# Performance work log

Hardware: AMD Instinct MI355X
Metric: run time of the kernel (lower is better)

## Reference

```python
import jax, jax.numpy as jnp
import numpy as np

BSZ, P, D, C = 16, 4096, 256, 512


def setup_inputs() -> dict:
    key = jax.random.key(0)
    k1, k2 = jax.random.split(key)
    x = jax.random.normal(k1, (BSZ, P, D), dtype=jnp.float32)
    kernels = jax.random.normal(k2, (C, D), dtype=jnp.float32) * 0.001
    return {"x": x, "kernels": kernels}


def reference(x, kernels):
    bsz, Pn, d = x.shape
    # (bsz, P, C) projection scores, ReLU'd
    scores = jax.nn.relu(jnp.einsum('bpd,cd->bpc', x, kernels))
    # per-channel argmax over positions -> (bsz, C)
    idx = jnp.argmax(scores, axis=1)
    # scatter_add each kernel row into its winning position
    b_idx = jnp.arange(bsz)[:, None]  # (bsz, 1) broadcast against (bsz, C)
    src = jnp.broadcast_to(kernels, (bsz,) + kernels.shape)  # (bsz, C, d)
    out = jnp.zeros((bsz, Pn, d), dtype=x.dtype).at[b_idx, idx].add(src)
    return out
```

## Files before the change

kernel.cpp:

```cpp
#include <hip/hip_runtime.h>
#include <cstddef>
#include <cstdint>

#define BSZ 16
#define PN  4096
#define DD  256
#define CC  512
#define TP  128
#define TC  64
#define NPT (PN / TP)
#define NCT (CC / TC)
#define NKC 8

typedef short bf16x8 __attribute__((ext_vector_type(8)));
typedef float f32x4  __attribute__((ext_vector_type(4)));

#define MEMFENCE() __asm__ __volatile__("" ::: "memory")
#define WAITCNT_VM0 0x1F70

struct Top2 { float v1, v2; int i1, i2; };

__device__ __forceinline__ void t2_insert(Top2& t, float v, int i) {
  if (v > t.v1 || (v == t.v1 && i < t.i1)) {
    t.v2 = t.v1; t.i2 = t.i1; t.v1 = v; t.i1 = i;
  } else if (v > t.v2 || (v == t.v2 && i < t.i2)) {
    t.v2 = v; t.i2 = i;
  }
}

__device__ __forceinline__ void split4(float4 v, uint2& hp, uint2& lp) {
  uint32_t u0 = __float_as_uint(v.x), u1 = __float_as_uint(v.y),
           u2 = __float_as_uint(v.z), u3 = __float_as_uint(v.w);
  float l0 = v.x - __uint_as_float(u0 & 0xffff0000u);
  float l1 = v.y - __uint_as_float(u1 & 0xffff0000u);
  float l2 = v.z - __uint_as_float(u2 & 0xffff0000u);
  float l3 = v.w - __uint_as_float(u3 & 0xffff0000u);
  hp.x = __builtin_amdgcn_perm(u1, u0, 0x07060302u);
  hp.y = __builtin_amdgcn_perm(u3, u2, 0x07060302u);
  lp.x = __builtin_amdgcn_perm(__float_as_uint(l1), __float_as_uint(l0), 0x07060302u);
  lp.y = __builtin_amdgcn_perm(__float_as_uint(l3), __float_as_uint(l2), 0x07060302u);
}

__device__ __forceinline__ void gld16(const void* gsrc, void* ldst) {
  __builtin_amdgcn_global_load_lds(
      (const __attribute__((address_space(1))) unsigned int*)gsrc,
      (__attribute__((address_space(3))) unsigned int*)ldst, 16, 0, 0);
}

__global__ __launch_bounds__(256) void convert_k_kernel(
    const float* __restrict__ kern, uint32_t* __restrict__ ks) {
  const int kc = blockIdx.x, ct = blockIdx.y;
  const size_t chunk = ((size_t)ct * NKC + kc) * 4096;
#pragma unroll
  for (int s0 = 0; s0 < 2; s0++) {
    int s  = threadIdx.x + s0 * 256;
    int fp = s >> 6, kg = (s >> 4) & 3, lr = s & 15;
    int r  = fp * 16 + lr, k0 = kg * 8;
    const float* src = kern + ((size_t)ct * 128 + r) * DD + kc * 32 + k0;
    float4 v0 = *(const float4*)src, v1 = *(const float4*)(src + 4);
    uint2 h0, l0, h1, l1; split4(v0, h0, l0); split4(v1, h1, l1);
    *(uint4*)&ks[chunk + (size_t)s * 4]        = make_uint4(h0.x, h0.y, h1.x, h1.y);
    *(uint4*)&ks[chunk + 2048 + (size_t)s * 4] = make_uint4(l0.x, l0.y, l1.x, l1.y);
  }
}

__global__ __launch_bounds__(256, 4) void score_kernel(
    const float* __restrict__ x, const uint32_t* __restrict__ ks,
    float2* __restrict__ pv2, uint32_t* __restrict__ pix) {

  __shared__ __align__(16) char lds[16384];

  const int d  = blockIdx.x;
  const int L  = (d & 7) * 512 + (d >> 3);
  const int ct = L & 7;
  const int pt = (L >> 3) & 31;
  const int b  = L >> 8;

  const int tid = threadIdx.x;
  const int lane = tid & 63, w = tid >> 6;
  const int lr = lane & 15, kg = lane >> 4;

  const char* ksbase = (const char*)ks + (size_t)(ct >> 1) * NKC * 16384 + (ct & 1) * 4096;
  const char* bsrc[2];
  bsrc[0] = ksbase + tid * 16;
  bsrc[1] = ksbase + 8192 + tid * 16;

  const char* xbase = (const char*)(x + ((size_t)b * PN + (size_t)pt * TP) * DD);
  const char* ap[2][2];
#pragma unroll
  for (int fp = 0; fp < 2; fp++)
#pragma unroll
    for (int h = 0; h < 2; h++)
      ap[fp][h] = xbase + (size_t)(w * 32 + fp * 16 + lr) * (DD * 4) + kg * 32 + h * 16;

  float4 abuf[2][2][2];

  auto issue = [&](int kc) {
    char* Bb = lds + (kc & 1) * 8192;
#pragma unroll
    for (int i = 0; i < 2; i++)
      gld16(bsrc[i] + kc * 16384, Bb + i * 4096 + tid * 16);
#pragma unroll
    for (int fp = 0; fp < 2; fp++)
#pragma unroll
      for (int h = 0; h < 2; h++)
        abuf[kc & 1][fp][h] = *(const float4*)(ap[fp][h] + kc * 128);
  };

  issue(0);
  MEMFENCE();
  __builtin_amdgcn_s_waitcnt(WAITCNT_VM0);
  __builtin_amdgcn_s_barrier();
  MEMFENCE();

  f32x4 acc[2][4];
#pragma unroll
  for (int i = 0; i < 2; i++)
#pragma unroll
    for (int j = 0; j < 4; j++) acc[i][j] = (f32x4)0.f;

#pragma unroll
  for (int kc = 0; kc < NKC; kc++) {
    if (kc + 1 < NKC) issue(kc + 1);

    bf16x8 Ah[2], Al[2];
#pragma unroll
    for (int fp = 0; fp < 2; fp++) {
      uint2 h0, l0, h1, l1;
      split4(abuf[kc & 1][fp][0], h0, l0);
      split4(abuf[kc & 1][fp][1], h1, l1);
      uint4 hh = make_uint4(h0.x, h0.y, h1.x, h1.y);
      uint4 ll = make_uint4(l0.x, l0.y, l1.x, l1.y);
      Ah[fp] = *(bf16x8*)&hh;
      Al[fp] = *(bf16x8*)&ll;
    }
    const char* Bb = lds + (kc & 1) * 8192;
#pragma unroll
    for (int fc = 0; fc < 4; fc++) {
      bf16x8 Bh = *(const bf16x8*)(Bb + fc * 1024 + lane * 16);
      bf16x8 Bl = *(const bf16x8*)(Bb + 4096 + fc * 1024 + lane * 16);
#pragma unroll
      for (int fp = 0; fp < 2; fp++) {
        acc[fp][fc] = __builtin_amdgcn_mfma_f32_16x16x32_bf16(Ah[fp], Bh, acc[fp][fc], 0, 0, 0);
        acc[fp][fc] = __builtin_amdgcn_mfma_f32_16x16x32_bf16(Ah[fp], Bl, acc[fp][fc], 0, 0, 0);
        acc[fp][fc] = __builtin_amdgcn_mfma_f32_16x16x32_bf16(Al[fp], Bh, acc[fp][fc], 0, 0, 0);
      }
    }
    MEMFENCE();
    __builtin_amdgcn_s_waitcnt(WAITCNT_VM0);
    __builtin_amdgcn_s_barrier();
    MEMFENCE();
  }

  float4* scratch = (float4*)lds;
  const int slot = w * 4 + kg;
#pragma unroll
  for (int fc = 0; fc < 4; fc++) {
    Top2 t; t.v1 = -1.f; t.v2 = -1.f; t.i1 = 0x7fffffff; t.i2 = 0x7fffffff;
#pragma unroll
    for (int fp = 0; fp < 2; fp++)
#pragma unroll
      for (int r = 0; r < 4; r++) {
        float v = acc[fp][fc][r]; v = v > 0.f ? v : 0.f;
        t2_insert(t, v, w * 32 + fp * 16 + kg * 4 + r);
      }
    scratch[slot * TC + fc * 16 + lr] =
        make_float4(t.v1, __int_as_float(t.i1), t.v2, __int_as_float(t.i2));
  }
  __syncthreads();

  if (tid < TC) {
    Top2 t; t.v1 = -1.f; t.v2 = -1.f; t.i1 = 0x7fffffff; t.i2 = 0x7fffffff;
#pragma unroll
    for (int s = 0; s < 16; s++) {
      float4 e = scratch[s * TC + tid];
      t2_insert(t, e.x, __float_as_int(e.y));
      t2_insert(t, e.z, __float_as_int(e.w));
    }
    int c = ct * TC + tid;
    size_t o = ((size_t)b * CC + c) * NPT + pt;
    uint32_t p1 = (uint32_t)(pt * TP + t.i1);
    uint32_t p2 = (uint32_t)(pt * TP + t.i2);
    pv2[o] = make_float2(t.v1, t.v2);
    pix[o] = (p1 << 16) | (p2 & 0xffffu);
  }
}

__global__ __launch_bounds__(64) void reduce_winner_kernel(
    const float2* __restrict__ pv2, const uint32_t* __restrict__ pix,
    const float* __restrict__ x, const float* __restrict__ kern,
    int* __restrict__ winner) {
  const int c = blockIdx.x, b = blockIdx.y;
  const int l = threadIdx.x;

  Top2 t; t.v1 = -1.f; t.v2 = -1.f; t.i1 = 0x7fffffff; t.i2 = 0x7fffffff;
  if (l < NPT) {
    size_t o = ((size_t)b * CC + c) * NPT + l;
    float2 v = pv2[o]; uint32_t ii = pix[o];
    t.v1 = v.x; t.v2 = v.y; t.i1 = (int)(ii >> 16); t.i2 = (int)(ii & 0xffffu);
  }
#pragma unroll
  for (int m = 1; m < 64; m <<= 1) {
    float uv1 = __shfl_xor(t.v1, m, 64);
    int   ui1 = __shfl_xor(t.i1, m, 64);
    float uv2 = __shfl_xor(t.v2, m, 64);
    int   ui2 = __shfl_xor(t.i2, m, 64);
    t2_insert(t, uv1, ui1);
    t2_insert(t, uv2, ui2);
  }

  int win = t.i1;
  if (t.v1 - t.v2 <= 1e-4f * t.v1 + 1e-5f) {
    const float4* x1 = (const float4*)(x + ((size_t)b * PN + t.i1) * DD);
    const float4* x2 = (const float4*)(x + ((size_t)b * PN + t.i2) * DD);
    const float4* kc = (const float4*)(kern + (size_t)c * DD);
    float4 a1 = x1[l], a2 = x2[l], k4 = kc[l];
    float s1 = a1.x * k4.x + a1.y * k4.y + a1.z * k4.z + a1.w * k4.w;
    float s2 = a2.x * k4.x + a2.y * k4.y + a2.z * k4.z + a2.w * k4.w;
#pragma unroll
    for (int m = 1; m < 64; m <<= 1) {
      s1 += __shfl_xor(s1, m, 64);
      s2 += __shfl_xor(s2, m, 64);
    }
    s1 = fmaxf(s1, 0.f); s2 = fmaxf(s2, 0.f);
    if (s2 > s1 || (s2 == s1 && t.i2 < t.i1)) win = t.i2;
  }
  if (l == 0) winner[(size_t)b * CC + c] = win;
}

__global__ __launch_bounds__(256) void write_out_kernel(
    const int* __restrict__ winner, const float* __restrict__ kern,
    float4* __restrict__ out) {
  __shared__ __align__(16) int wrow[CC];
  const int b = blockIdx.y;
  const int tid = threadIdx.x, lane = tid & 63, w = tid >> 6;
  const int p = blockIdx.x * 4 + w;

  *(int2*)&wrow[tid * 2] = *(const int2*)&winner[(size_t)b * CC + tid * 2];
  __syncthreads();

  int4 w0 = *(const int4*)&wrow[lane * 8];
  int4 w1 = *(const int4*)&wrow[lane * 8 + 4];
  int wv[8] = {w0.x, w0.y, w0.z, w0.w, w1.x, w1.y, w1.z, w1.w};

  float4 acc = make_float4(0.f, 0.f, 0.f, 0.f);
#pragma unroll
  for (int j = 0; j < 8; j++) {
    unsigned long long m = __ballot(wv[j] == p);
    while (m) {
      int bit = __ffsll((long long)m) - 1; m &= m - 1;
      int c = bit * 8 + j;
      float4 kv = ((const float4*)(kern + (size_t)c * DD))[lane];
      acc.x += kv.x; acc.y += kv.y; acc.z += kv.z; acc.w += kv.w;
    }
  }
  out[((size_t)b * PN + p) * 64 + lane] = acc;
}

extern "C" void kernel_launch(void* const* d_in, const int* in_sizes, int n_in,
                              void* d_out, int out_size, void* d_ws, size_t ws_size,
                              hipStream_t stream) {
  const float* x    = (const float*)d_in[0];
  const float* kern = (const float*)d_in[1];
  float* out = (float*)d_out;

  char* ws = (char*)d_ws;
  float2*   pv2 = (float2*)ws;
  uint32_t* pix = (uint32_t*)(ws + (size_t)BSZ * CC * NPT * sizeof(float2));
  uint32_t* ks  = (uint32_t*)(ws + 3u * 1024 * 1024);
  int*      win = (int*)(ws + 3u * 1024 * 1024 + 512u * 1024);

  convert_k_kernel<<<dim3(NKC, CC / 128), 256, 0, stream>>>(kern, ks);

  score_kernel<<<dim3(NCT * NPT * BSZ), 256, 0, stream>>>(x, ks, pv2, pix);

  reduce_winner_kernel<<<dim3(CC, BSZ), 64, 0, stream>>>(pv2, pix, x, kern, win);

  write_out_kernel<<<dim3(PN / 4, BSZ), 256, 0, stream>>>(win, kern, (float4*)out);
}
```

Before: 196.2 us.

## Double score tile height, triple-buffer B in LDS, and widen reduce blocks

Doubles the position tile in the score kernel to 256 rows, so each wave computes 64 rows and every B fragment read from LDS feeds twice as many MFMAs. It also splits the A register prefetch from the B LDS prefetch, triple-buffers B two chunks ahead with partial vmcnt waits, and raises wave priority around the MFMA block. The reduce kernel now packs four channels per 256-thread block, and the convert kernel spreads its work across a third grid dimension. The cost is more accumulator registers (launch bounds drop to 2 blocks per SM) and half as many score blocks, which may lower occupancy and load balance.

```diff
diff --git a/kernel.cpp b/kernel.cpp
--- a/kernel.cpp
+++ b/kernel.cpp
@@ -6,7 +6,7 @@
 #define PN  4096
 #define DD  256
 #define CC  512
-#define TP  128
+#define TP  256
 #define TC  64
 #define NPT (PN / TP)
 #define NCT (CC / TC)
@@ -17,6 +17,7 @@
 
 #define MEMFENCE() __asm__ __volatile__("" ::: "memory")
 #define WAITCNT_VM0 0x1F70
+#define WAITCNT_VM2 0x1F72
 
 struct Top2 { float v1, v2; int i1, i2; };
 
@@ -51,30 +52,27 @@
     const float* __restrict__ kern, uint32_t* __restrict__ ks) {
   const int kc = blockIdx.x, ct = blockIdx.y;
   const size_t chunk = ((size_t)ct * NKC + kc) * 4096;
-#pragma unroll
-  for (int s0 = 0; s0 < 2; s0++) {
-    int s  = threadIdx.x + s0 * 256;
-    int fp = s >> 6, kg = (s >> 4) & 3, lr = s & 15;
-    int r  = fp * 16 + lr, k0 = kg * 8;
-    const float* src = kern + ((size_t)ct * 128 + r) * DD + kc * 32 + k0;
-    float4 v0 = *(const float4*)src, v1 = *(const float4*)(src + 4);
-    uint2 h0, l0, h1, l1; split4(v0, h0, l0); split4(v1, h1, l1);
-    *(uint4*)&ks[chunk + (size_t)s * 4]        = make_uint4(h0.x, h0.y, h1.x, h1.y);
-    *(uint4*)&ks[chunk + 2048 + (size_t)s * 4] = make_uint4(l0.x, l0.y, l1.x, l1.y);
-  }
-}
-
-__global__ __launch_bounds__(256, 4) void score_kernel(
+  int s  = threadIdx.x + blockIdx.z * 256;
+  int fp = s >> 6, kg = (s >> 4) & 3, lr = s & 15;
+  int r  = fp * 16 + lr, k0 = kg * 8;
+  const float* src = kern + ((size_t)ct * 128 + r) * DD + kc * 32 + k0;
+  float4 v0 = *(const float4*)src, v1 = *(const float4*)(src + 4);
+  uint2 h0, l0, h1, l1; split4(v0, h0, l0); split4(v1, h1, l1);
+  *(uint4*)&ks[chunk + (size_t)s * 4]        = make_uint4(h0.x, h0.y, h1.x, h1.y);
+  *(uint4*)&ks[chunk + 2048 + (size_t)s * 4] = make_uint4(l0.x, l0.y, l1.x, l1.y);
+}
+
+__global__ __launch_bounds__(256, 2) void score_kernel(
     const float* __restrict__ x, const uint32_t* __restrict__ ks,
     float2* __restrict__ pv2, uint32_t* __restrict__ pix) {
 
-  __shared__ __align__(16) char lds[16384];
+  __shared__ __align__(16) char lds[24576];
 
   const int d  = blockIdx.x;
-  const int L  = (d & 7) * 512 + (d >> 3);
+  const int L  = (d & 7) * 256 + (d >> 3);
   const int ct = L & 7;
-  const int pt = (L >> 3) & 31;
-  const int b  = L >> 8;
+  const int pt = (L >> 3) & 15;
+  const int b  = L >> 7;
 
   const int tid = threadIdx.x;
   const int lane = tid & 63, w = tid >> 6;
@@ -86,46 +84,52 @@
   bsrc[1] = ksbase + 8192 + tid * 16;
 
   const char* xbase = (const char*)(x + ((size_t)b * PN + (size_t)pt * TP) * DD);
-  const char* ap[2][2];
-#pragma unroll
-  for (int fp = 0; fp < 2; fp++)
+  const char* ap[4][2];
+#pragma unroll
+  for (int fp = 0; fp < 4; fp++)
 #pragma unroll
     for (int h = 0; h < 2; h++)
-      ap[fp][h] = xbase + (size_t)(w * 32 + fp * 16 + lr) * (DD * 4) + kg * 32 + h * 16;
-
-  float4 abuf[2][2][2];
-
-  auto issue = [&](int kc) {
-    char* Bb = lds + (kc & 1) * 8192;
-#pragma unroll
-    for (int i = 0; i < 2; i++)
-      gld16(bsrc[i] + kc * 16384, Bb + i * 4096 + tid * 16);
-#pragma unroll
-    for (int fp = 0; fp < 2; fp++)
+      ap[fp][h] = xbase + (size_t)(w * 64 + fp * 16 + lr) * (DD * 4) + kg * 32 + h * 16;
+
+  float4 abuf[2][4][2];
+
+  auto loadA = [&](int kc) {
+#pragma unroll
+    for (int fp = 0; fp < 4; fp++)
 #pragma unroll
       for (int h = 0; h < 2; h++)
         abuf[kc & 1][fp][h] = *(const float4*)(ap[fp][h] + kc * 128);
   };
-
-  issue(0);
+  auto issueB = [&](int kc) {
+    char* Bb = lds + (kc % 3) * 8192;
+#pragma unroll
+    for (int i = 0; i < 2; i++)
+      gld16(bsrc[i] + kc * 16384, Bb + i * 4096 + tid * 16);
+  };
+
+  loadA(0);
+  issueB(0);
+  issueB(1);
   MEMFENCE();
-  __builtin_amdgcn_s_waitcnt(WAITCNT_VM0);
+  __builtin_amdgcn_s_waitcnt(WAITCNT_VM2);
   __builtin_amdgcn_s_barrier();
   MEMFENCE();
 
-  f32x4 acc[2][4];
-#pragma unroll
-  for (int i = 0; i < 2; i++)
+  f32x4 acc[4][4];
+#pragma unroll
+  for (int i = 0; i < 4; i++)
 #pragma unroll
     for (int j = 0; j < 4; j++) acc[i][j] = (f32x4)0.f;
 
 #pragma unroll
   for (int kc = 0; kc < NKC; kc++) {
-    if (kc + 1 < NKC) issue(kc + 1);
-
-    bf16x8 Ah[2], Al[2];
-#pragma unroll
-    for (int fp = 0; fp < 2; fp++) {
+    if (kc + 1 < NKC) loadA(kc + 1);
+    if (kc + 2 < NKC) issueB(kc + 2);
+    __builtin_amdgcn_sched_barrier(0);
+
+    bf16x8 Ah[4], Al[4];
+#pragma unroll
+    for (int fp = 0; fp < 4; fp++) {
       uint2 h0, l0, h1, l1;
       split4(abuf[kc & 1][fp][0], h0, l0);
       split4(abuf[kc & 1][fp][1], h1, l1);
@@ -134,20 +138,26 @@
       Ah[fp] = *(bf16x8*)&hh;
       Al[fp] = *(bf16x8*)&ll;
     }
-    const char* Bb = lds + (kc & 1) * 8192;
+    const char* Bb = lds + (kc % 3) * 8192;
+    __builtin_amdgcn_s_setprio(1);
 #pragma unroll
     for (int fc = 0; fc < 4; fc++) {
       bf16x8 Bh = *(const bf16x8*)(Bb + fc * 1024 + lane * 16);
       bf16x8 Bl = *(const bf16x8*)(Bb + 4096 + fc * 1024 + lane * 16);
 #pragma unroll
-      for (int fp = 0; fp < 2; fp++) {
+      for (int fp = 0; fp < 4; fp++) {
         acc[fp][fc] = __builtin_amdgcn_mfma_f32_16x16x32_bf16(Ah[fp], Bh, acc[fp][fc], 0, 0, 0);
         acc[fp][fc] = __builtin_amdgcn_mfma_f32_16x16x32_bf16(Ah[fp], Bl, acc[fp][fc], 0, 0, 0);
         acc[fp][fc] = __builtin_amdgcn_mfma_f32_16x16x32_bf16(Al[fp], Bh, acc[fp][fc], 0, 0, 0);
       }
     }
+    __builtin_amdgcn_s_setprio(0);
     MEMFENCE();
-    __builtin_amdgcn_s_waitcnt(WAITCNT_VM0);
+    if (kc + 2 < NKC) {
+      __builtin_amdgcn_s_waitcnt(WAITCNT_VM2);
+    } else if (kc + 1 < NKC) {
+      __builtin_amdgcn_s_waitcnt(WAITCNT_VM0);
+    }
     __builtin_amdgcn_s_barrier();
     MEMFENCE();
   }
@@ -158,11 +168,11 @@
   for (int fc = 0; fc < 4; fc++) {
     Top2 t; t.v1 = -1.f; t.v2 = -1.f; t.i1 = 0x7fffffff; t.i2 = 0x7fffffff;
 #pragma unroll
-    for (int fp = 0; fp < 2; fp++)
+    for (int fp = 0; fp < 4; fp++)
 #pragma unroll
       for (int r = 0; r < 4; r++) {
         float v = acc[fp][fc][r]; v = v > 0.f ? v : 0.f;
-        t2_insert(t, v, w * 32 + fp * 16 + kg * 4 + r);
+        t2_insert(t, v, w * 64 + fp * 16 + kg * 4 + r);
       }
     scratch[slot * TC + fc * 16 + lr] =
         make_float4(t.v1, __int_as_float(t.i1), t.v2, __int_as_float(t.i2));
@@ -186,12 +196,13 @@
   }
 }
 
-__global__ __launch_bounds__(64) void reduce_winner_kernel(
+__global__ __launch_bounds__(256) void reduce_winner_kernel(
     const float2* __restrict__ pv2, const uint32_t* __restrict__ pix,
     const float* __restrict__ x, const float* __restrict__ kern,
     int* __restrict__ winner) {
-  const int c = blockIdx.x, b = blockIdx.y;
-  const int l = threadIdx.x;
+  const int b = blockIdx.y;
+  const int c = blockIdx.x * 4 + (threadIdx.x >> 6);
+  const int l = threadIdx.x & 63;
 
   Top2 t; t.v1 = -1.f; t.v2 = -1.f; t.i1 = 0x7fffffff; t.i2 = 0x7fffffff;
   if (l < NPT) {
@@ -266,15 +277,15 @@
 
   char* ws = (char*)d_ws;
   float2*   pv2 = (float2*)ws;
-  uint32_t* pix = (uint32_t*)(ws + (size_t)BSZ * CC * NPT * sizeof(float2));
+  uint32_t* pix = (uint32_t*)(ws + 2u * 1024 * 1024);
   uint32_t* ks  = (uint32_t*)(ws + 3u * 1024 * 1024);
   int*      win = (int*)(ws + 3u * 1024 * 1024 + 512u * 1024);
 
-  convert_k_kernel<<<dim3(NKC, CC / 128), 256, 0, stream>>>(kern, ks);
+  convert_k_kernel<<<dim3(NKC, CC / 128, 2), 256, 0, stream>>>(kern, ks);
 
   score_kernel<<<dim3(NCT * NPT * BSZ), 256, 0, stream>>>(x, ks, pv2, pix);
 
-  reduce_winner_kernel<<<dim3(CC, BSZ), 64, 0, stream>>>(pv2, pix, x, kern, win);
+  reduce_winner_kernel<<<dim3(CC / 4, BSZ), 256, 0, stream>>>(pv2, pix, x, kern, win);
 
   write_out_kernel<<<dim3(PN / 4, BSZ), 256, 0, stream>>>(win, kern, (float4*)out);
 }
```

New measurement: 186.6 us. 4.9% less time.
